# Optimization experiments

Measured on AMD Instinct MI355X. Metric: run time of the kernel, lower is better.

## Reference

```python
import jax, jax.numpy as jnp
import numpy as np

B, CIN, COUT, H, W, KK = 1, 32, 64, 181, 360, 4
NNZ_PER, NNZ_PER1 = 9, 4


def _make_psi(rng, K, H, W, nnz_per):
    # Sparse DISCO basis in COO form for longitude 0 (shift-invariant in lon).
    E = K * H * nnz_per
    seg = np.repeat(np.arange(K * H, dtype=np.int32), nnz_per)  # k*H + ho
    ho = seg % H
    dlat = rng.integers(-1, 2, size=E).astype(np.int32)
    hi = np.clip(ho + dlat, 0, H - 1).astype(np.int32)
    wi = (rng.integers(-1, 2, size=E).astype(np.int32)) % W
    vals = (rng.normal(size=E) * 0.2).astype(np.float32)
    return seg, hi, wi, vals


def setup_inputs() -> dict:
    rng = np.random.default_rng(0)
    key = jax.random.key(0)
    ks = jax.random.split(key, 5)
    x = jax.random.normal(ks[0], (B, CIN, H, W), dtype=jnp.float32)
    # spherical quadrature weights: sin(colatitude) * cell area
    theta = np.linspace(0.0, np.pi, H)
    qw = (np.sin(theta) * (np.pi / (H - 1)) * (2.0 * np.pi / W)).astype(np.float32)
    qw = np.maximum(qw, 1e-8).reshape(H, 1)
    seg, hi, wi, vals = _make_psi(rng, KK, H, W, NNZ_PER)
    seg1, hi1, wi1, vals1 = _make_psi(rng, 1, H, W, NNZ_PER1)
    w_depth = jax.random.normal(ks[1], (CIN, KK), dtype=jnp.float32) / np.sqrt(KK)
    w_point = jax.random.normal(ks[2], (COUT, CIN), dtype=jnp.float32) / np.sqrt(CIN)
    bias = jax.random.normal(ks[3], (COUT,), dtype=jnp.float32) * 0.02
    return {
        "x": x,
        "quad_w": jnp.asarray(qw),
        "vals": jnp.asarray(vals),
        "seg": jnp.asarray(seg),
        "hi": jnp.asarray(hi),
        "wi": jnp.asarray(wi),
        "w_depth": w_depth,
        "vals1": jnp.asarray(vals1),
        "seg1": jnp.asarray(seg1),
        "hi1": jnp.asarray(hi1),
        "wi1": jnp.asarray(wi1),
        "w_point": w_point,
        "bias": bias,
        "K": KK,
    }


def _disco_contract(x, vals, seg, hi, wi, K):
    # x: [B,C,H,W]; COO psi at lon 0; out[b,c,k,ho,wo] =
    #   sum_{e: seg[e]==k*H+ho} vals[e] * x[b,c,hi[e],(wi[e]+wo) mod W]
    Bq, C, Hq, Wq = x.shape
    rows = x[:, :, hi, :]                                        # [B,C,E,W]
    col = (wi[:, None] + jnp.arange(Wq, dtype=wi.dtype)[None, :]) % Wq  # [E,W]
    rolled = jnp.take_along_axis(rows, col[None, None, :, :], axis=3)   # [B,C,E,W]
    weighted = rolled * vals[None, None, :, None]
    out = jax.ops.segment_sum(weighted.transpose(2, 0, 1, 3), seg,
                              num_segments=K * Hq)               # [K*H,B,C,W]
    return out.reshape(K, Hq, Bq, C, Wq).transpose(2, 3, 0, 1, 4)  # [B,C,K,H,W]


def reference(x, quad_w, vals, seg, hi, wi, w_depth, vals1, seg1, hi1, wi1,
              w_point, bias, K):
    # depthwise DISCO conv (groups=C_in, no bias)
    xq = x * quad_w                                   # quadrature weighting
    xd = _disco_contract(xq, vals, seg, hi, wi, K)    # [B,C,K,H,W]
    y = jnp.einsum("ck,bckhw->bchw", w_depth, xd)     # per-channel K mix
    # pointwise DISCO conv (kernel_shape=1) = CLinear
    yq = y * quad_w
    z = _disco_contract(yq, vals1, seg1, hi1, wi1, 1)[:, :, 0]  # [B,C,H,W]
    out = jnp.einsum("oc,bchw->bohw", w_point, z) + bias[None, :, None, None]
    return out
```

## Files before the change

kernel.cpp:

```cpp
#include <hip/hip_runtime.h>


#define H_    181
#define W_    360
#define CIN_  32
#define COUT_ 64
#define K_    4
#define NNZ_  9
#define NNZ1_ 4
#define HW_   (H_*W_)
#define NT_   (NNZ1_*K_*NNZ_)

__global__ __launch_bounds__(512) void sepconv_one(
    const float* __restrict__ x, const float* __restrict__ quad_w,
    const float* __restrict__ vals, const int* __restrict__ hi,
    const int* __restrict__ wi, const float* __restrict__ w_depth,
    const float* __restrict__ vals1, const int* __restrict__ hi1,
    const int* __restrict__ wi1, const float* __restrict__ w_point,
    const float* __restrict__ bias, float* __restrict__ out)
{
    const int bx = blockIdx.x;
    const int h  = (bx & 7) * 23 + (bx >> 3);
    if (h >= H_) return;
    const int seg = blockIdx.y;
    const int w0  = seg * 64;
    const int pxn = (seg == 5) ? 40 : 64;
    const int gn  = pxn >> 2;
    const int tid = threadIdx.x;

    __shared__ float Tval[NT_];
    __shared__ int   Tbin[NT_];
    __shared__ float S[K_][25];
    __shared__ float C[CIN_][25];
    __shared__ float zs[64][33];

    const int g = tid & 15;
    const int c = tid >> 4;
    const bool act = (g < gn);

    int rowoff[5];
    #pragma unroll
    for (int rb = 0; rb < 5; ++rb) {
        int r = h - 2 + rb;
        r = (r < 0) ? 0 : ((r > H_ - 1) ? H_ - 1 : r);
        rowoff[rb] = r * W_;
    }

    const int bw = w0 + g * 4;
    const int cA = (bw + W_ - 4) % W_;
    const int cB = bw;
    const int cC = (bw + 4) % W_;

    float4 L[15];
    if (act) {
        const float* xc = x + c * HW_;
        #pragma unroll
        for (int rb = 0; rb < 5; ++rb) {
            const float* xr = xc + rowoff[rb];
            L[rb * 3 + 0] = *(const float4*)(xr + cA);
            L[rb * 3 + 1] = *(const float4*)(xr + cB);
            L[rb * 3 + 2] = *(const float4*)(xr + cC);
        }
    }

    if (tid < NT_) {
        const int a   = tid / 36;
        const int rem = tid - a * 36;
        const int k   = rem / 9;
        const int j   = rem - k * 9;
        const int e1  = h * NNZ1_ + a;
        const int m   = hi1[e1];
        const int w1  = wi1[e1];
        const int d1  = (w1 == 1) ? 1 : ((w1 == 0) ? 0 : -1);
        const int e   = (k * H_ + m) * NNZ_ + j;
        const int r   = hi[e];
        const int ww  = wi[e];
        const int d   = (ww == 1) ? 1 : ((ww == 0) ? 0 : -1);
        Tval[tid] = vals1[e1] * quad_w[m] * vals[e] * quad_w[r];
        Tbin[tid] = (r - h + 2) * 5 + (d1 + d + 2);
    }
    __syncthreads();

    if (tid < K_ * 25) {
        const int k   = tid / 25;
        const int bin = tid - k * 25;
        float s = 0.f;
        #pragma unroll
        for (int a = 0; a < NNZ1_; ++a)
            #pragma unroll
            for (int j = 0; j < NNZ_; ++j) {
                const int t2 = a * 36 + k * 9 + j;
                if (Tbin[t2] == bin) s += Tval[t2];
            }
        S[k][bin] = s;
    }
    __syncthreads();

    if (tid < CIN_ * 25) {
        const int cc = tid / 25, bin = tid - cc * 25;
        float acc = 0.f;
        #pragma unroll
        for (int k = 0; k < K_; ++k) acc += w_depth[cc * K_ + k] * S[k][bin];
        C[cc][bin] = acc;
    }
    if (tid + 512 < CIN_ * 25) {
        const int i2 = tid + 512;
        const int cc = i2 / 25, bin = i2 - cc * 25;
        float acc = 0.f;
        #pragma unroll
        for (int k = 0; k < K_; ++k) acc += w_depth[cc * K_ + k] * S[k][bin];
        C[cc][bin] = acc;
    }
    __syncthreads();

    if (act) {
        const float* Cc = &C[c][0];
        float a0 = 0.f, a1 = 0.f, a2 = 0.f, a3 = 0.f;
        #pragma unroll
        for (int rb = 0; rb < 5; ++rb) {
            const float4 vA = L[rb * 3 + 0];
            const float4 vB = L[rb * 3 + 1];
            const float4 vC = L[rb * 3 + 2];
            const float k0 = Cc[rb * 5 + 0], k1 = Cc[rb * 5 + 1],
                        k2 = Cc[rb * 5 + 2], k3 = Cc[rb * 5 + 3],
                        k4 = Cc[rb * 5 + 4];
            a0 += k0 * vA.z + k1 * vA.w + k2 * vB.x + k3 * vB.y + k4 * vB.z;
            a1 += k0 * vA.w + k1 * vB.x + k2 * vB.y + k3 * vB.z + k4 * vB.w;
            a2 += k0 * vB.x + k1 * vB.y + k2 * vB.z + k3 * vB.w + k4 * vC.x;
            a3 += k0 * vB.y + k1 * vB.z + k2 * vB.w + k3 * vC.x + k4 * vC.y;
        }
        const int p = g * 4;
        zs[p + 0][c] = a0;
        zs[p + 1][c] = a1;
        zs[p + 2][c] = a2;
        zs[p + 3][c] = a3;
    }
    __syncthreads();

    const int j  = tid & 63;
    const int oh = tid >> 6;
    if (j < pxn) {
        float zr[CIN_];
        #pragma unroll
        for (int cc = 0; cc < CIN_; ++cc) zr[cc] = zs[j][cc];

        const float* wp = w_point + oh * 8 * CIN_;
        float* op = out + oh * 8 * HW_ + h * W_ + w0 + j;
        #pragma unroll
        for (int oo = 0; oo < 8; ++oo) {
            float acc = bias[oh * 8 + oo];
            #pragma unroll
            for (int cc = 0; cc < CIN_; ++cc)
                acc += wp[oo * CIN_ + cc] * zr[cc];
            op[oo * HW_] = acc;
        }
    }
}

extern "C" void kernel_launch(void* const* d_in, const int* in_sizes, int n_in,
                              void* d_out, int out_size, void* d_ws, size_t ws_size,
                              hipStream_t stream) {
    const float* x       = (const float*)d_in[0];
    const float* quad_w  = (const float*)d_in[1];
    const float* vals    = (const float*)d_in[2];
    const int*   hi      = (const int*)d_in[4];
    const int*   wi      = (const int*)d_in[5];
    const float* w_depth = (const float*)d_in[6];
    const float* vals1   = (const float*)d_in[7];
    const int*   hi1     = (const int*)d_in[9];
    const int*   wi1     = (const int*)d_in[10];
    const float* w_point = (const float*)d_in[11];
    const float* bias    = (const float*)d_in[12];

    sepconv_one<<<dim3(184, 6), 512, 0, stream>>>(
        x, quad_w, vals, hi, wi, w_depth, vals1, hi1, wi1,
        w_point, bias, (float*)d_out);
}
```

Before: 116.1 us.

## Convert to persistent grid with software-pipelined prefetch of next tile

Replaces the 184x6 one-tile-per-block grid with 512 persistent blocks that each loop over several (row, segment) tiles within a latitude band. While the pointwise output stage of the current tile runs, the block issues the global loads of x and decodes the sparse basis for the next tile, so load latency overlaps compute. The cost is extra barriers per iteration, more live registers (launch bounds 512,4), and serial per-block work that may reduce parallelism for a small grid.

```diff
diff --git a/kernel.cpp b/kernel.cpp
--- a/kernel.cpp
+++ b/kernel.cpp
@@ -11,7 +11,12 @@
 #define HW_   (H_*W_)
 #define NT_   (NNZ1_*K_*NNZ_)
 
-__global__ __launch_bounds__(512) void sepconv_one(
+__device__ __forceinline__ void tile_hs(int band, int t, int& h, int& seg) {
+    h   = band * 23 + t / 6;
+    seg = t - (t / 6) * 6;
+}
+
+__global__ __launch_bounds__(512, 4) void sepconv_persist(
     const float* __restrict__ x, const float* __restrict__ quad_w,
     const float* __restrict__ vals, const int* __restrict__ hi,
     const int* __restrict__ wi, const float* __restrict__ w_depth,
@@ -19,14 +24,17 @@
     const int* __restrict__ wi1, const float* __restrict__ w_point,
     const float* __restrict__ bias, float* __restrict__ out)
 {
-    const int bx = blockIdx.x;
-    const int h  = (bx & 7) * 23 + (bx >> 3);
-    if (h >= H_) return;
-    const int seg = blockIdx.y;
-    const int w0  = seg * 64;
-    const int pxn = (seg == 5) ? 40 : 64;
-    const int gn  = pxn >> 2;
-    const int tid = threadIdx.x;
+    const int bx     = blockIdx.x;
+    const int band   = bx & 7;
+    const int within = bx >> 3;
+    const int rows   = (band < 7) ? 23 : 20;
+    const int nt     = rows * 6;
+    const int tid    = threadIdx.x;
+
+    const int g = tid & 15;
+    const int c = tid >> 4;
+    const int j  = tid & 63;
+    const int oh = tid >> 6;
 
     __shared__ float Tval[NT_];
     __shared__ int   Tbin[NT_];
@@ -34,126 +42,149 @@
     __shared__ float C[CIN_][25];
     __shared__ float zs[64][33];
 
-    const int g = tid & 15;
-    const int c = tid >> 4;
-    const bool act = (g < gn);
-
-    int rowoff[5];
-    #pragma unroll
-    for (int rb = 0; rb < 5; ++rb) {
-        int r = h - 2 + rb;
-        r = (r < 0) ? 0 : ((r > H_ - 1) ? H_ - 1 : r);
-        rowoff[rb] = r * W_;
-    }
-
-    const int bw = w0 + g * 4;
-    const int cA = (bw + W_ - 4) % W_;
-    const int cB = bw;
-    const int cC = (bw + 4) % W_;
+    auto decode = [&](int h) {
+        if (tid < NT_) {
+            const int a   = tid / 36;
+            const int rem = tid - a * 36;
+            const int k   = rem / 9;
+            const int jj  = rem - k * 9;
+            const int e1  = h * NNZ1_ + a;
+            const int m   = hi1[e1];
+            const int w1  = wi1[e1];
+            const int d1  = (w1 == 1) ? 1 : ((w1 == 0) ? 0 : -1);
+            const int e   = (k * H_ + m) * NNZ_ + jj;
+            const int r   = hi[e];
+            const int ww  = wi[e];
+            const int d   = (ww == 1) ? 1 : ((ww == 0) ? 0 : -1);
+            Tval[tid] = vals1[e1] * quad_w[m] * vals[e] * quad_w[r];
+            Tbin[tid] = (r - h + 2) * 5 + (d1 + d + 2);
+        }
+    };
+    auto build_S = [&]() {
+        if (tid < K_ * 25) {
+            const int k   = tid / 25;
+            const int bin = tid - k * 25;
+            float s = 0.f;
+            #pragma unroll
+            for (int a = 0; a < NNZ1_; ++a)
+                #pragma unroll
+                for (int jj = 0; jj < NNZ_; ++jj) {
+                    const int t2 = a * 36 + k * 9 + jj;
+                    if (Tbin[t2] == bin) s += Tval[t2];
+                }
+            S[k][bin] = s;
+        }
+    };
+    auto build_C = [&]() {
+        for (int i = tid; i < CIN_ * 25; i += 512) {
+            const int cc = i / 25, bin = i - cc * 25;
+            float acc = 0.f;
+            #pragma unroll
+            for (int k = 0; k < K_; ++k)
+                acc += w_depth[cc * K_ + k] * S[k][bin];
+            C[cc][bin] = acc;
+        }
+    };
+    auto load_x = [&](int h, int seg, float4* L, bool& act) {
+        const int pxn = (seg == 5) ? 40 : 64;
+        act = (g < (pxn >> 2));
+        if (act) {
+            const int bw = seg * 64 + g * 4;
+            const int cA = (bw + W_ - 4) % W_;
+            const int cB = bw;
+            const int cC = (bw + 4) % W_;
+            const float* xc = x + c * HW_;
+            #pragma unroll
+            for (int rb = 0; rb < 5; ++rb) {
+                int r = h - 2 + rb;
+                r = (r < 0) ? 0 : ((r > H_ - 1) ? H_ - 1 : r);
+                const float* xr = xc + r * W_;
+                L[rb * 3 + 0] = *(const float4*)(xr + cA);
+                L[rb * 3 + 1] = *(const float4*)(xr + cB);
+                L[rb * 3 + 2] = *(const float4*)(xr + cC);
+            }
+        }
+    };
+
+    int t = within;
+    if (t >= nt) return;
+    int h0, s0;  tile_hs(band, t, h0, s0);
 
     float4 L[15];
-    if (act) {
-        const float* xc = x + c * HW_;
-        #pragma unroll
-        for (int rb = 0; rb < 5; ++rb) {
-            const float* xr = xc + rowoff[rb];
-            L[rb * 3 + 0] = *(const float4*)(xr + cA);
-            L[rb * 3 + 1] = *(const float4*)(xr + cB);
-            L[rb * 3 + 2] = *(const float4*)(xr + cC);
-        }
-    }
-
-    if (tid < NT_) {
-        const int a   = tid / 36;
-        const int rem = tid - a * 36;
-        const int k   = rem / 9;
-        const int j   = rem - k * 9;
-        const int e1  = h * NNZ1_ + a;
-        const int m   = hi1[e1];
-        const int w1  = wi1[e1];
-        const int d1  = (w1 == 1) ? 1 : ((w1 == 0) ? 0 : -1);
-        const int e   = (k * H_ + m) * NNZ_ + j;
-        const int r   = hi[e];
-        const int ww  = wi[e];
-        const int d   = (ww == 1) ? 1 : ((ww == 0) ? 0 : -1);
-        Tval[tid] = vals1[e1] * quad_w[m] * vals[e] * quad_w[r];
-        Tbin[tid] = (r - h + 2) * 5 + (d1 + d + 2);
-    }
+    bool act;
+    load_x(h0, s0, L, act);
+    decode(h0);
     __syncthreads();
-
-    if (tid < K_ * 25) {
-        const int k   = tid / 25;
-        const int bin = tid - k * 25;
-        float s = 0.f;
-        #pragma unroll
-        for (int a = 0; a < NNZ1_; ++a)
-            #pragma unroll
-            for (int j = 0; j < NNZ_; ++j) {
-                const int t2 = a * 36 + k * 9 + j;
-                if (Tbin[t2] == bin) s += Tval[t2];
+    build_S();
+    __syncthreads();
+    build_C();
+    __syncthreads();
+
+    while (true) {
+        const int tn    = t + 64;
+        const bool more = (tn < nt);
+        int hn = h0, sn = s0;
+        if (more) tile_hs(band, tn, hn, sn);
+
+        if (act) {
+            const float* Cc = &C[c][0];
+            float a0 = 0.f, a1 = 0.f, a2 = 0.f, a3 = 0.f;
+            #pragma unroll
+            for (int rb = 0; rb < 5; ++rb) {
+                const float4 vA = L[rb * 3 + 0];
+                const float4 vB = L[rb * 3 + 1];
+                const float4 vC = L[rb * 3 + 2];
+                const float k0 = Cc[rb * 5 + 0], k1 = Cc[rb * 5 + 1],
+                            k2 = Cc[rb * 5 + 2], k3 = Cc[rb * 5 + 3],
+                            k4 = Cc[rb * 5 + 4];
+                a0 += k0 * vA.z + k1 * vA.w + k2 * vB.x + k3 * vB.y + k4 * vB.z;
+                a1 += k0 * vA.w + k1 * vB.x + k2 * vB.y + k3 * vB.z + k4 * vB.w;
+                a2 += k0 * vB.x + k1 * vB.y + k2 * vB.z + k3 * vB.w + k4 * vC.x;
+                a3 += k0 * vB.y + k1 * vB.z + k2 * vB.w + k3 * vC.x + k4 * vC.y;
             }
-        S[k][bin] = s;
-    }
-    __syncthreads();
-
-    if (tid < CIN_ * 25) {
-        const int cc = tid / 25, bin = tid - cc * 25;
-        float acc = 0.f;
-        #pragma unroll
-        for (int k = 0; k < K_; ++k) acc += w_depth[cc * K_ + k] * S[k][bin];
-        C[cc][bin] = acc;
-    }
-    if (tid + 512 < CIN_ * 25) {
-        const int i2 = tid + 512;
-        const int cc = i2 / 25, bin = i2 - cc * 25;
-        float acc = 0.f;
-        #pragma unroll
-        for (int k = 0; k < K_; ++k) acc += w_depth[cc * K_ + k] * S[k][bin];
-        C[cc][bin] = acc;
-    }
-    __syncthreads();
-
-    if (act) {
-        const float* Cc = &C[c][0];
-        float a0 = 0.f, a1 = 0.f, a2 = 0.f, a3 = 0.f;
-        #pragma unroll
-        for (int rb = 0; rb < 5; ++rb) {
-            const float4 vA = L[rb * 3 + 0];
-            const float4 vB = L[rb * 3 + 1];
-            const float4 vC = L[rb * 3 + 2];
-            const float k0 = Cc[rb * 5 + 0], k1 = Cc[rb * 5 + 1],
-                        k2 = Cc[rb * 5 + 2], k3 = Cc[rb * 5 + 3],
-                        k4 = Cc[rb * 5 + 4];
-            a0 += k0 * vA.z + k1 * vA.w + k2 * vB.x + k3 * vB.y + k4 * vB.z;
-            a1 += k0 * vA.w + k1 * vB.x + k2 * vB.y + k3 * vB.z + k4 * vB.w;
-            a2 += k0 * vB.x + k1 * vB.y + k2 * vB.z + k3 * vB.w + k4 * vC.x;
-            a3 += k0 * vB.y + k1 * vB.z + k2 * vB.w + k3 * vC.x + k4 * vC.y;
-        }
-        const int p = g * 4;
-        zs[p + 0][c] = a0;
-        zs[p + 1][c] = a1;
-        zs[p + 2][c] = a2;
-        zs[p + 3][c] = a3;
-    }
-    __syncthreads();
-
-    const int j  = tid & 63;
-    const int oh = tid >> 6;
-    if (j < pxn) {
-        float zr[CIN_];
-        #pragma unroll
-        for (int cc = 0; cc < CIN_; ++cc) zr[cc] = zs[j][cc];
-
-        const float* wp = w_point + oh * 8 * CIN_;
-        float* op = out + oh * 8 * HW_ + h * W_ + w0 + j;
-        #pragma unroll
-        for (int oo = 0; oo < 8; ++oo) {
-            float acc = bias[oh * 8 + oo];
-            #pragma unroll
-            for (int cc = 0; cc < CIN_; ++cc)
-                acc += wp[oo * CIN_ + cc] * zr[cc];
-            op[oo * HW_] = acc;
-        }
+            const int p = g * 4;
+            zs[p + 0][c] = a0;
+            zs[p + 1][c] = a1;
+            zs[p + 2][c] = a2;
+            zs[p + 3][c] = a3;
+        }
+
+        bool actn = false;
+        if (more) load_x(hn, sn, L, actn);
+
+        __syncthreads();
+
+        if (more) decode(hn);
+
+        {
+            const int w0  = s0 * 64;
+            const int pxn = (s0 == 5) ? 40 : 64;
+            if (j < pxn) {
+                float zr[CIN_];
+                #pragma unroll
+                for (int cc = 0; cc < CIN_; ++cc) zr[cc] = zs[j][cc];
+                const float* wp = w_point + oh * 8 * CIN_;
+                float* op = out + oh * 8 * HW_ + h0 * W_ + w0 + j;
+                #pragma unroll
+                for (int oo = 0; oo < 8; ++oo) {
+                    float acc = bias[oh * 8 + oo];
+                    #pragma unroll
+                    for (int cc = 0; cc < CIN_; ++cc)
+                        acc += wp[oo * CIN_ + cc] * zr[cc];
+                    op[oo * HW_] = acc;
+                }
+            }
+        }
+
+        if (!more) break;
+
+        __syncthreads();
+        build_S();
+        __syncthreads();
+        build_C();
+        __syncthreads();
+
+        t = tn; h0 = hn; s0 = sn; act = actn;
     }
 }
 
@@ -172,7 +203,7 @@
     const float* w_point = (const float*)d_in[11];
     const float* bias    = (const float*)d_in[12];
 
-    sepconv_one<<<dim3(184, 6), 512, 0, stream>>>(
+    sepconv_persist<<<512, 512, 0, stream>>>(
         x, quad_w, vals, hi, wi, w_depth, vals1, hi1, wi1,
         w_point, bias, (float*)d_out);
 }
```

Measured after the change: 118.0 us. Within noise of the previous version (+1.6%).
